# Optimization experiments

Hardware: AMD Instinct MI355X
Metric: run time of the kernel (lower is better)

The kernel has to match this reference:

```python
import jax, jax.numpy as jnp
import numpy as np

N_HIDDEN = 100  # module-level global n_hidden in source
LN_EPS = 1e-5


def _layernorm(x, g, b):
    mu = jnp.mean(x, axis=-1, keepdims=True)
    var = jnp.mean(jnp.square(x - mu), axis=-1, keepdims=True)
    return (x - mu) * jax.lax.rsqrt(var + LN_EPS) * g + b


def setup_inputs() -> dict:
    key = jax.random.key(0)
    B, T, C, H = 8, 1024, 768, 12
    D = C // H  # head_size = 64
    ks = jax.random.split(key, 12)
    s_qkv = 1.0 / np.sqrt(C)
    s_ff1 = 1.0 / np.sqrt(C)
    s_ff2 = 1.0 / np.sqrt(N_HIDDEN)
    return {
        "x": jax.random.normal(ks[0], (B, T, C), dtype=jnp.float32),
        # per-head K/Q/V projections stacked: [H, C, D]
        "Wq": jax.random.uniform(ks[1], (H, C, D), jnp.float32, -s_qkv, s_qkv),
        "Wk": jax.random.uniform(ks[2], (H, C, D), jnp.float32, -s_qkv, s_qkv),
        "Wv": jax.random.uniform(ks[3], (H, C, D), jnp.float32, -s_qkv, s_qkv),
        "Wproj": jax.random.uniform(ks[4], (C, C), jnp.float32, -s_qkv, s_qkv),
        "bproj": jnp.zeros((C,), jnp.float32),
        "ln1_g": jnp.ones((C,), jnp.float32),
        "ln1_b": jnp.zeros((C,), jnp.float32),
        "W1": jax.random.uniform(ks[5], (C, N_HIDDEN), jnp.float32, -s_ff1, s_ff1),
        "b1": jnp.zeros((N_HIDDEN,), jnp.float32),
        "W2": jax.random.uniform(ks[6], (N_HIDDEN, C), jnp.float32, -s_ff2, s_ff2),
        "b2": jnp.zeros((C,), jnp.float32),
        "ln2_g": jnp.ones((C,), jnp.float32),
        "ln2_b": jnp.zeros((C,), jnp.float32),
    }


def reference(x, Wq, Wk, Wv, Wproj, bproj, ln1_g, ln1_b, W1, b1, W2, b2, ln2_g, ln2_b):
    B, T, C = x.shape
    # batched-over-heads QKV (source does a Python loop per head; same math)
    q = jnp.einsum('btc,hcd->bhtd', x, Wq)
    k = jnp.einsum('btc,hcd->bhtd', x, Wk)
    v = jnp.einsum('btc,hcd->bhtd', x, Wv)
    # NOTE: source scales by C**-0.5 where C = n_embd (not head_size)
    wei = jnp.einsum('bhtd,bhsd->bhts', q, k) * (C ** -0.5)
    wei = jax.nn.softmax(wei, axis=-1)  # attn_maps, returned
    out = jnp.einsum('bhts,bhsd->bhtd', wei, v)
    out = out.transpose(0, 2, 1, 3).reshape(B, T, C)  # concat heads
    attn_out = out @ Wproj + bproj
    h = _layernorm(x + attn_out, ln1_g, ln1_b)
    ff = jax.nn.relu(h @ W1 + b1) @ W2 + b2
    y = _layernorm(h + ff, ln2_g, ln2_b)
    return (wei, y)
```

## Files before the change

### kernel.cpp

```cpp
#include <hip/hip_runtime.h>
#include <hip/hip_bf16.h>
#include <cstdint>

typedef __bf16 bf16_t;
typedef __bf16 bf16x8 __attribute__((ext_vector_type(8)));
typedef __bf16 bf16x4 __attribute__((ext_vector_type(4)));
typedef float f32x4 __attribute__((ext_vector_type(4)));

#define B_ 8
#define T_ 1024
#define C_ 768
#define H_ 12
#define D_ 64
#define NTOK 8192
#define NHID_PAD 128
#define SCALE 0.03608439182435161f
#define WEI_ELEMS 100663296ull

__device__ __forceinline__ f32x4 mfma16(bf16x8 a, bf16x8 b, f32x4 c) {
    return __builtin_amdgcn_mfma_f32_16x16x32_bf16(a, b, c, 0, 0, 0);
}

typedef const unsigned int __attribute__((address_space(1)))* gaddr_t;
typedef unsigned int __attribute__((address_space(3)))* laddr_t;
__device__ __forceinline__ void gload16(const bf16_t* g, bf16_t* l) {
    __builtin_amdgcn_global_load_lds((gaddr_t)g, (laddr_t)l, 16, 0, 0);
}

__global__ __launch_bounds__(256) void k_prep(const float* __restrict__ x, bf16_t* __restrict__ xb,
                                              const float* __restrict__ Wq, const float* __restrict__ Wk,
                                              const float* __restrict__ Wv, bf16_t* __restrict__ wqkvt,
                                              const float* __restrict__ Wproj, bf16_t* __restrict__ wprojt,
                                              const float* __restrict__ W1, bf16_t* __restrict__ w1t,
                                              const float* __restrict__ W2, bf16_t* __restrict__ w2t) {
    int blk = blockIdx.x;
    int tid = threadIdx.x;
    if (blk < 6144) {
        int i = blk * 256 + tid;
        const float4 v = reinterpret_cast<const float4*>(x)[i];
        bf16x4 o;
        o.x = (bf16_t)v.x; o.y = (bf16_t)v.y; o.z = (bf16_t)v.z; o.w = (bf16_t)v.w;
        *reinterpret_cast<bf16x4*>(xb + 4 * i) = o;
    } else if (blk < 13056) {
        int idx = (blk - 6144) * 256 + tid;
        int row = idx / C_, c = idx - row * C_;
        int p = row / C_;
        int hd = row - p * C_;
        int h = hd >> 6, d = hd & 63;
        const float* W = (p == 0) ? Wq : (p == 1 ? Wk : Wv);
        wqkvt[idx] = (bf16_t)W[((size_t)h * C_ + c) * D_ + d];
    } else if (blk < 15360) {
        int idx = (blk - 13056) * 256 + tid;
        int n = idx / C_, k = idx - n * C_;
        wprojt[idx] = (bf16_t)Wproj[(size_t)k * C_ + n];
    } else if (blk < 15744) {
        int idx = (blk - 15360) * 256 + tid;
        int n = idx / C_, k = idx - n * C_;
        w1t[idx] = (bf16_t)((n < 100) ? W1[(size_t)k * 100 + n] : 0.0f);
    } else {
        int idx = (blk - 15744) * 256 + tid;
        int n = idx / NHID_PAD, k = idx & (NHID_PAD - 1);
        w2t[idx] = (bf16_t)((k < 100) ? W2[(size_t)k * C_ + n] : 0.0f);
    }
}

__device__ __forceinline__ void gemm_core(bf16_t* As, bf16_t* Bs,
                                          const bf16_t* __restrict__ A, int lda,
                                          const bf16_t* __restrict__ B, int ldb,
                                          int K, int bm, int bn, f32x4 acc[4][4]) {
    const int tid = threadIdx.x;
    const int wave = tid >> 6, lane = tid & 63;
    const int q = lane >> 4, ln = lane & 15;
    const int wm = (wave >> 1) * 64, wn = (wave & 1) * 64;

    const int c0 = wave * 2;
    const int srow = c0 * 16 + (lane >> 2);
    const int kg = (lane & 3) * 8;
    const bf16_t* Ap0 = A + (size_t)(bm + srow) * lda + kg;
    const bf16_t* Ap1 = A + (size_t)(bm + srow + 16) * lda + kg;
    const bf16_t* Bp0 = B + (size_t)(bn + srow) * ldb + kg;
    const bf16_t* Bp1 = B + (size_t)(bn + srow + 16) * ldb + kg;

    const int nt = K >> 5;
    gload16(Ap0, As + c0 * 512);
    gload16(Ap1, As + (c0 + 1) * 512);
    gload16(Bp0, Bs + c0 * 512);
    gload16(Bp1, Bs + (c0 + 1) * 512);
    int cur = 0;
    for (int t = 0; t < nt; ++t) {
        __syncthreads();
        if (t + 1 < nt) {
            int k0 = (t + 1) << 5;
            bf16_t* Ad = As + (cur ^ 1) * 4096;
            bf16_t* Bd = Bs + (cur ^ 1) * 4096;
            gload16(Ap0 + k0, Ad + c0 * 512);
            gload16(Ap1 + k0, Ad + (c0 + 1) * 512);
            gload16(Bp0 + k0, Bd + c0 * 512);
            gload16(Bp1 + k0, Bd + (c0 + 1) * 512);
        }
        const bf16_t* Ab = As + cur * 4096;
        const bf16_t* Bb = Bs + cur * 4096;
        bf16x8 af[4], bfr[4];
#pragma unroll
        for (int i = 0; i < 4; ++i)
            af[i] = *reinterpret_cast<const bf16x8*>(&Ab[(wm + i * 16 + ln) * 32 + q * 8]);
#pragma unroll
        for (int j = 0; j < 4; ++j)
            bfr[j] = *reinterpret_cast<const bf16x8*>(&Bb[(wn + j * 16 + ln) * 32 + q * 8]);
#pragma unroll
        for (int i = 0; i < 4; ++i)
#pragma unroll
            for (int j = 0; j < 4; ++j)
                acc[i][j] = mfma16(af[i], bfr[j], acc[i][j]);
        cur ^= 1;
    }
}

#define EPI_PROLOG(bm, bn)                                      \
    const int lane = threadIdx.x & 63;                          \
    const int wave = threadIdx.x >> 6;                          \
    const int q = lane >> 4, ln = lane & 15;                    \
    const int row0 = (bm) + (wave >> 1) * 64;                   \
    const int col0 = (bn) + (wave & 1) * 64;

__global__ __launch_bounds__(256) void k_gemm_qkv(const bf16_t* __restrict__ xb,
                                                  const bf16_t* __restrict__ wqkvt,
                                                  bf16_t* __restrict__ qb,
                                                  bf16_t* __restrict__ kb,
                                                  bf16_t* __restrict__ vt) {
    __shared__ __align__(16) bf16_t As[2 * 4096];
    __shared__ __align__(16) bf16_t Bs[2 * 4096];
    const int bid = blockIdx.x;
    if (bid < 768) {
        const int bx = bid % 12, by = bid / 12;
        f32x4 acc[4][4] = {};
        gemm_core(As, Bs, xb, C_, wqkvt, C_, C_, by * 128, bx * 128, acc);
        EPI_PROLOG(by * 128, bx * 128)
#pragma unroll
        for (int i = 0; i < 4; ++i)
#pragma unroll
            for (int j = 0; j < 4; ++j)
#pragma unroll
                for (int r = 0; r < 4; ++r) {
                    int grow = row0 + i * 16 + q * 4 + r;
                    int gcol = col0 + j * 16 + ln;
                    int p = (gcol >= C_) ? 1 : 0;
                    int c = gcol - p * C_;
                    int h = c >> 6, d = c & 63;
                    int b = grow >> 10, t = grow & 1023;
                    bf16_t* dst = p ? kb : qb;
                    dst[(((size_t)b * H_ + h) * T_ + t) * D_ + d] = (bf16_t)acc[i][j][r];
                }
    } else {
        const int b2 = bid - 768;
        const int bx = b2 & 63, by = b2 >> 6;
        f32x4 acc[4][4] = {};
        gemm_core(As, Bs, wqkvt + (size_t)1536 * C_, C_, xb, C_, C_, by * 128, bx * 128, acc);
        EPI_PROLOG(by * 128, bx * 128)
#pragma unroll
        for (int i = 0; i < 4; ++i)
#pragma unroll
            for (int j = 0; j < 4; ++j)
#pragma unroll
                for (int r = 0; r < 4; ++r) {
                    int grow = row0 + i * 16 + q * 4 + r;
                    int gcol = col0 + j * 16 + ln;
                    int h = grow >> 6, d = grow & 63;
                    int b = gcol >> 10, t = gcol & 1023;
                    vt[(((size_t)b * H_ + h) * D_ + d) * T_ + t] = (bf16_t)acc[i][j][r];
                }
    }
}

__global__ __launch_bounds__(256) void k_gemm_proj(const bf16_t* __restrict__ A,
                                                   const bf16_t* __restrict__ Bm,
                                                   const float* __restrict__ bias,
                                                   float* __restrict__ out) {
    __shared__ __align__(16) bf16_t As[2 * 4096];
    __shared__ __align__(16) bf16_t Bs[2 * 4096];
    f32x4 acc[4][4] = {};
    gemm_core(As, Bs, A, C_, Bm, C_, C_, blockIdx.y * 128, blockIdx.x * 128, acc);
    EPI_PROLOG(blockIdx.y * 128, blockIdx.x * 128)
#pragma unroll
    for (int i = 0; i < 4; ++i)
#pragma unroll
        for (int j = 0; j < 4; ++j)
#pragma unroll
            for (int r = 0; r < 4; ++r) {
                int grow = row0 + i * 16 + q * 4 + r;
                int gcol = col0 + j * 16 + ln;
                out[(size_t)grow * C_ + gcol] = acc[i][j][r] + bias[gcol];
            }
}

__global__ __launch_bounds__(256) void k_ff(const bf16_t* __restrict__ hbb,
                                            const bf16_t* __restrict__ w1t,
                                            const float* __restrict__ b1,
                                            const bf16_t* __restrict__ w2t,
                                            const float* __restrict__ b2,
                                            float* __restrict__ out) {
    __shared__ __align__(16) bf16_t As[2 * 4096];
    __shared__ __align__(16) bf16_t Bs[2 * 4096];
    __shared__ __align__(16) bf16_t Hs[128 * 128];
    const int bm = blockIdx.y * 128;
    f32x4 acc[4][4] = {};
    gemm_core(As, Bs, hbb, C_, w1t, C_, C_, bm, 0, acc);

    const int tid = threadIdx.x;
    const int wave = tid >> 6, lane = tid & 63;
    const int q = lane >> 4, ln = lane & 15;
    const int wm = (wave >> 1) * 64, wn = (wave & 1) * 64;
#pragma unroll
    for (int i = 0; i < 4; ++i)
#pragma unroll
        for (int j = 0; j < 4; ++j)
#pragma unroll
            for (int r = 0; r < 4; ++r) {
                int row = wm + i * 16 + q * 4 + r;
                int col = wn + j * 16 + ln;
                float v = acc[i][j][r] + ((col < 100) ? b1[col] : 0.0f);
                v = fmaxf(v, 0.0f);
                Hs[(row * 128 + col) ^ ((row & 7) << 3)] = (bf16_t)v;
            }
    __syncthreads();

#pragma unroll
    for (int nt2 = 0; nt2 < 2; ++nt2) {
        const int cb = blockIdx.x * 256 + nt2 * 128;
        f32x4 a2[4][4] = {};
#pragma unroll
        for (int k0 = 0; k0 < 128; k0 += 32) {
            bf16x8 af[4], bfr[4];
#pragma unroll
            for (int i = 0; i < 4; ++i) {
                int row = wm + i * 16 + ln;
                af[i] = *reinterpret_cast<const bf16x8*>(
                    &Hs[(row * 128 + k0 + q * 8) ^ ((row & 7) << 3)]);
            }
#pragma unroll
            for (int j = 0; j < 4; ++j)
                bfr[j] = *reinterpret_cast<const bf16x8*>(
                    &w2t[(size_t)(cb + wn + j * 16 + ln) * NHID_PAD + k0 + q * 8]);
#pragma unroll
            for (int i = 0; i < 4; ++i)
#pragma unroll
                for (int j = 0; j < 4; ++j)
                    a2[i][j] = mfma16(af[i], bfr[j], a2[i][j]);
        }
#pragma unroll
        for (int i = 0; i < 4; ++i)
#pragma unroll
            for (int j = 0; j < 4; ++j)
#pragma unroll
                for (int r = 0; r < 4; ++r) {
                    int grow = bm + wm + i * 16 + q * 4 + r;
                    int gcol = cb + wn + j * 16 + ln;
                    out[(size_t)grow * C_ + gcol] = a2[i][j][r] + b2[gcol];
                }
    }
}

__global__ __launch_bounds__(256, 3) void k_attn(const bf16_t* __restrict__ qb,
                                                 const bf16_t* __restrict__ kb,
                                                 const bf16_t* __restrict__ vt,
                                                 float* __restrict__ wei,
                                                 bf16_t* __restrict__ attn) {
    __shared__ __align__(16) bf16_t Ps[16 * 1032];
    __shared__ float redm[4][16];
    __shared__ float reds[4][16];

    const int tid = threadIdx.x;
    const int w = tid >> 6, lane = tid & 63;
    const int qq = lane >> 4, ln = lane & 15;
    const int bh = blockIdx.y;
    const int b = bh / H_, h = bh - b * H_;
    const int t0 = blockIdx.x * 16;
    const size_t bhbase = (size_t)bh * (T_ * D_);

    const bf16_t* qp = qb + bhbase + (size_t)(t0 + ln) * D_ + qq * 8;
    const bf16x8 aq0 = *reinterpret_cast<const bf16x8*>(qp);
    const bf16x8 aq1 = *reinterpret_cast<const bf16x8*>(qp + 32);

    f32x4 sacc[16] = {};
    const bf16_t* kp = kb + bhbase + (size_t)(w * 256 + ln) * D_ + qq * 8;
#pragma unroll
    for (int j = 0; j < 16; ++j) {
        bf16x8 b0 = *reinterpret_cast<const bf16x8*>(kp + j * 16 * D_);
        bf16x8 b1 = *reinterpret_cast<const bf16x8*>(kp + j * 16 * D_ + 32);
        sacc[j] = mfma16(aq0, b0, sacc[j]);
        sacc[j] = mfma16(aq1, b1, sacc[j]);
    }

    float mx[4];
#pragma unroll
    for (int r = 0; r < 4; ++r) {
        float m = sacc[0][r];
#pragma unroll
        for (int j = 1; j < 16; ++j) m = fmaxf(m, sacc[j][r]);
#pragma unroll
        for (int off = 1; off < 16; off <<= 1) m = fmaxf(m, __shfl_xor(m, off));
        mx[r] = m;
    }
    if (ln == 0) {
#pragma unroll
        for (int r = 0; r < 4; ++r) redm[w][qq * 4 + r] = mx[r];
    }
    __syncthreads();
#pragma unroll
    for (int r = 0; r < 4; ++r) {
        int row = qq * 4 + r;
        mx[r] = fmaxf(fmaxf(redm[0][row], redm[1][row]),
                      fmaxf(redm[2][row], redm[3][row]));
    }

    float rs[4] = {0.0f, 0.0f, 0.0f, 0.0f};
#pragma unroll
    for (int j = 0; j < 16; ++j)
#pragma unroll
        for (int r = 0; r < 4; ++r) {
            float p = __expf((sacc[j][r] - mx[r]) * SCALE);
            sacc[j][r] = p;
            rs[r] += p;
        }
#pragma unroll
    for (int r = 0; r < 4; ++r)
#pragma unroll
        for (int off = 1; off < 16; off <<= 1) rs[r] += __shfl_xor(rs[r], off);
    if (ln == 0) {
#pragma unroll
        for (int r = 0; r < 4; ++r) reds[w][qq * 4 + r] = rs[r];
    }
    __syncthreads();
    float inv[4];
#pragma unroll
    for (int r = 0; r < 4; ++r) {
        int row = qq * 4 + r;
        inv[r] = 1.0f / (reds[0][row] + reds[1][row] + reds[2][row] + reds[3][row]);
    }

    float* wbase = wei + ((size_t)bh << 20) + (size_t)t0 * T_ + w * 256 + ln;
#pragma unroll
    for (int r = 0; r < 4; ++r) {
        int row = qq * 4 + r;
        float* wr = wbase + (size_t)row * T_;
        bf16_t* pr = &Ps[row * 1032 + w * 256 + ln];
#pragma unroll
        for (int j = 0; j < 16; ++j) {
            float p = sacc[j][r] * inv[r];
            __builtin_nontemporal_store(p, wr + j * 16);
            pr[j * 16] = (bf16_t)p;
        }
    }
    __syncthreads();

    f32x4 oacc = {};
    const bf16_t* vp = vt + (size_t)bh * (D_ * T_) + (size_t)(w * 16 + ln) * T_ + qq * 8;
#pragma unroll
    for (int ks = 0; ks < 32; ++ks) {
        bf16x8 a = *reinterpret_cast<const bf16x8*>(&Ps[ln * 1032 + ks * 32 + qq * 8]);
        bf16x8 bv = *reinterpret_cast<const bf16x8*>(vp + ks * 32);
        oacc = mfma16(a, bv, oacc);
    }
#pragma unroll
    for (int r = 0; r < 4; ++r) {
        int trow = t0 + qq * 4 + r;
        attn[((size_t)b * T_ + trow) * C_ + h * D_ + w * 16 + ln] = (bf16_t)oacc[r];
    }
}

__global__ __launch_bounds__(256) void k_ln(const float* __restrict__ a,
                                            const float* __restrict__ bsrc,
                                            const float* __restrict__ g,
                                            const float* __restrict__ beta,
                                            float* __restrict__ of,
                                            bf16_t* __restrict__ ob,
                                            int streaming) {
    int row = blockIdx.x;
    int tid = threadIdx.x;
    const float* pa = a + (size_t)row * C_;
    const float* pb = bsrc + (size_t)row * C_;
    float v[3];
    float s = 0.0f, s2 = 0.0f;
#pragma unroll
    for (int u = 0; u < 3; ++u) {
        int c = tid + u * 256;
        v[u] = pa[c] + pb[c];
        s += v[u];
        s2 += v[u] * v[u];
    }
#pragma unroll
    for (int off = 32; off; off >>= 1) {
        s += __shfl_down(s, off);
        s2 += __shfl_down(s2, off);
    }
    __shared__ float ws[4], ws2[4];
    if ((tid & 63) == 0) { ws[tid >> 6] = s; ws2[tid >> 6] = s2; }
    __syncthreads();
    s = ws[0] + ws[1] + ws[2] + ws[3];
    s2 = ws2[0] + ws2[1] + ws2[2] + ws2[3];
    float mu = s * (1.0f / C_);
    float var = s2 * (1.0f / C_) - mu * mu;
    float ri = rsqrtf(var + 1e-5f);
#pragma unroll
    for (int u = 0; u < 3; ++u) {
        int c = tid + u * 256;
        float y = (v[u] - mu) * ri * g[c] + beta[c];
        if (streaming) __builtin_nontemporal_store(y, &of[(size_t)row * C_ + c]);
        else of[(size_t)row * C_ + c] = y;
        if (ob) ob[(size_t)row * C_ + c] = (bf16_t)y;
    }
}

extern "C" void kernel_launch(void* const* d_in, const int* in_sizes, int n_in,
                              void* d_out, int out_size, void* d_ws, size_t ws_size,
                              hipStream_t stream) {
    const float* x     = (const float*)d_in[0];
    const float* Wq    = (const float*)d_in[1];
    const float* Wk    = (const float*)d_in[2];
    const float* Wv    = (const float*)d_in[3];
    const float* Wproj = (const float*)d_in[4];
    const float* bproj = (const float*)d_in[5];
    const float* ln1g  = (const float*)d_in[6];
    const float* ln1b  = (const float*)d_in[7];
    const float* W1    = (const float*)d_in[8];
    const float* b1    = (const float*)d_in[9];
    const float* W2    = (const float*)d_in[10];
    const float* b2    = (const float*)d_in[11];
    const float* ln2g  = (const float*)d_in[12];
    const float* ln2b  = (const float*)d_in[13];

    char* ws = (char*)d_ws;
    bf16_t* xb     = (bf16_t*)(ws + 0);
    bf16_t* wqkvt  = (bf16_t*)(ws + 12582912);
    bf16_t* qbuf   = (bf16_t*)(ws + 16121856);
    bf16_t* kbuf   = (bf16_t*)(ws + 28704768);
    bf16_t* vtb    = (bf16_t*)(ws + 41287680);
    bf16_t* attnb  = (bf16_t*)(ws + 53870592);
    bf16_t* wprojt = (bf16_t*)(ws + 66453504);
    float*  projb  = (float*)(ws + 67633152);
    float*  hbuf   = (float*)(ws + 92798976);
    bf16_t* w1t    = (bf16_t*)(ws + 120061952);
    bf16_t* w2t    = (bf16_t*)(ws + 120258560);
    bf16_t* hbb    = xb;
    float*  ffb    = projb;

    float* wei = (float*)d_out;
    float* y   = (float*)d_out + WEI_ELEMS;

    k_prep<<<16128, 256, 0, stream>>>(x, xb, Wq, Wk, Wv, wqkvt, Wproj, wprojt,
                                      W1, w1t, W2, w2t);
    k_gemm_qkv<<<1152, 256, 0, stream>>>(xb, wqkvt, qbuf, kbuf, vtb);
    k_attn<<<dim3(64, 96), 256, 0, stream>>>(qbuf, kbuf, vtb, wei, attnb);
    k_gemm_proj<<<dim3(6, 64), 256, 0, stream>>>(attnb, wprojt, bproj, projb);
    k_ln<<<8192, 256, 0, stream>>>(x, projb, ln1g, ln1b, hbuf, hbb, 0);
    k_ff<<<dim3(3, 64), 256, 0, stream>>>(hbb, w1t, b1, w2t, b2, ffb);
    k_ln<<<8192, 256, 0, stream>>>(hbuf, ffb, ln2g, ln2b, y, (bf16_t*)nullptr, 1);

    (void)in_sizes; (void)n_in; (void)out_size; (void)ws_size;
}
```

Baseline: 726.5 us.

## Remap block indices for XCD-local L2 reuse and persist attention blocks over query tiles

Block IDs in the QKV, projection and FF GEMMs are remapped so that consecutive blocks on the same XCD (bid&7) share row panels, aiming to improve per-XCD L2 reuse of A/B tiles. The attention kernel drops from 6144 to 768 blocks, each looping over 8 query tiles of one batch-head, so K/V reuse stays within an XCD's L2. An extra __syncthreads is added in k_ff, presumably to guard LDS reuse. Cost: fewer attention blocks means less parallelism and latency hiding per CU, and loop-carried syncs are added.

```diff
diff --git a/kernel.cpp b/kernel.cpp
--- a/kernel.cpp
+++ b/kernel.cpp
@@ -12,7 +12,6 @@
 #define C_ 768
 #define H_ 12
 #define D_ 64
-#define NTOK 8192
 #define NHID_PAD 128
 #define SCALE 0.03608439182435161f
 #define WEI_ELEMS 100663296ull
@@ -132,7 +131,8 @@
     __shared__ __align__(16) bf16_t Bs[2 * 4096];
     const int bid = blockIdx.x;
     if (bid < 768) {
-        const int bx = bid % 12, by = bid / 12;
+        const int xcd = bid & 7, i2 = bid >> 3;
+        const int by = xcd * 8 + i2 / 12, bx = i2 % 12;
         f32x4 acc[4][4] = {};
         gemm_core(As, Bs, xb, C_, wqkvt, C_, C_, by * 128, bx * 128, acc);
         EPI_PROLOG(by * 128, bx * 128)
@@ -153,7 +153,8 @@
                 }
     } else {
         const int b2 = bid - 768;
-        const int bx = b2 & 63, by = b2 >> 6;
+        const int xcd = b2 & 7, i2 = b2 >> 3;
+        const int bx = xcd * 8 + i2 / 6, by = i2 % 6;
         f32x4 acc[4][4] = {};
         gemm_core(As, Bs, wqkvt + (size_t)1536 * C_, C_, xb, C_, C_, by * 128, bx * 128, acc);
         EPI_PROLOG(by * 128, bx * 128)
@@ -178,9 +179,12 @@
                                                    float* __restrict__ out) {
     __shared__ __align__(16) bf16_t As[2 * 4096];
     __shared__ __align__(16) bf16_t Bs[2 * 4096];
+    const int bid = blockIdx.x;
+    const int xcd = bid & 7, i2 = bid >> 3;
+    const int by = xcd * 8 + i2 / 6, bx = i2 % 6;
     f32x4 acc[4][4] = {};
-    gemm_core(As, Bs, A, C_, Bm, C_, C_, blockIdx.y * 128, blockIdx.x * 128, acc);
-    EPI_PROLOG(blockIdx.y * 128, blockIdx.x * 128)
+    gemm_core(As, Bs, A, C_, Bm, C_, C_, by * 128, bx * 128, acc);
+    EPI_PROLOG(by * 128, bx * 128)
 #pragma unroll
     for (int i = 0; i < 4; ++i)
 #pragma unroll
@@ -202,7 +206,10 @@
     __shared__ __align__(16) bf16_t As[2 * 4096];
     __shared__ __align__(16) bf16_t Bs[2 * 4096];
     __shared__ __align__(16) bf16_t Hs[128 * 128];
-    const int bm = blockIdx.y * 128;
+    const int bid = blockIdx.x;
+    const int xcd = bid & 7, i2 = bid >> 3;
+    const int fy = xcd * 8 + i2 / 3, fx = i2 % 3;
+    const int bm = fy * 128;
     f32x4 acc[4][4] = {};
     gemm_core(As, Bs, hbb, C_, w1t, C_, C_, bm, 0, acc);
 
@@ -210,6 +217,7 @@
     const int wave = tid >> 6, lane = tid & 63;
     const int q = lane >> 4, ln = lane & 15;
     const int wm = (wave >> 1) * 64, wn = (wave & 1) * 64;
+    __syncthreads();
 #pragma unroll
     for (int i = 0; i < 4; ++i)
 #pragma unroll
@@ -226,7 +234,7 @@
 
 #pragma unroll
     for (int nt2 = 0; nt2 < 2; ++nt2) {
-        const int cb = blockIdx.x * 256 + nt2 * 128;
+        const int cb = fx * 256 + nt2 * 128;
         f32x4 a2[4][4] = {};
 #pragma unroll
         for (int k0 = 0; k0 < 128; k0 += 32) {
@@ -272,99 +280,106 @@
     const int tid = threadIdx.x;
     const int w = tid >> 6, lane = tid & 63;
     const int qq = lane >> 4, ln = lane & 15;
-    const int bh = blockIdx.y;
+    const int bid = blockIdx.x;
+    const int tg = bid / 96;
+    const int bh = bid % 96;
     const int b = bh / H_, h = bh - b * H_;
-    const int t0 = blockIdx.x * 16;
     const size_t bhbase = (size_t)bh * (T_ * D_);
 
-    const bf16_t* qp = qb + bhbase + (size_t)(t0 + ln) * D_ + qq * 8;
-    const bf16x8 aq0 = *reinterpret_cast<const bf16x8*>(qp);
-    const bf16x8 aq1 = *reinterpret_cast<const bf16x8*>(qp + 32);
-
-    f32x4 sacc[16] = {};
-    const bf16_t* kp = kb + bhbase + (size_t)(w * 256 + ln) * D_ + qq * 8;
-#pragma unroll
-    for (int j = 0; j < 16; ++j) {
-        bf16x8 b0 = *reinterpret_cast<const bf16x8*>(kp + j * 16 * D_);
-        bf16x8 b1 = *reinterpret_cast<const bf16x8*>(kp + j * 16 * D_ + 32);
-        sacc[j] = mfma16(aq0, b0, sacc[j]);
-        sacc[j] = mfma16(aq1, b1, sacc[j]);
-    }
-
-    float mx[4];
-#pragma unroll
-    for (int r = 0; r < 4; ++r) {
-        float m = sacc[0][r];
-#pragma unroll
-        for (int j = 1; j < 16; ++j) m = fmaxf(m, sacc[j][r]);
-#pragma unroll
-        for (int off = 1; off < 16; off <<= 1) m = fmaxf(m, __shfl_xor(m, off));
-        mx[r] = m;
-    }
-    if (ln == 0) {
-#pragma unroll
-        for (int r = 0; r < 4; ++r) redm[w][qq * 4 + r] = mx[r];
-    }
-    __syncthreads();
-#pragma unroll
-    for (int r = 0; r < 4; ++r) {
-        int row = qq * 4 + r;
-        mx[r] = fmaxf(fmaxf(redm[0][row], redm[1][row]),
-                      fmaxf(redm[2][row], redm[3][row]));
-    }
-
-    float rs[4] = {0.0f, 0.0f, 0.0f, 0.0f};
-#pragma unroll
-    for (int j = 0; j < 16; ++j)
+    for (int u = 0; u < 8; ++u) {
+        const int t0 = (tg * 8 + u) * 16;
+        __syncthreads();
+
+        const bf16_t* qp = qb + bhbase + (size_t)(t0 + ln) * D_ + qq * 8;
+        const bf16x8 aq0 = *reinterpret_cast<const bf16x8*>(qp);
+        const bf16x8 aq1 = *reinterpret_cast<const bf16x8*>(qp + 32);
+
+        f32x4 sacc[16] = {};
+        const bf16_t* kp = kb + bhbase + (size_t)(w * 256 + ln) * D_ + qq * 8;
+#pragma unroll
+        for (int j = 0; j < 16; ++j) {
+            bf16x8 b0 = *reinterpret_cast<const bf16x8*>(kp + j * 16 * D_);
+            bf16x8 b1 = *reinterpret_cast<const bf16x8*>(kp + j * 16 * D_ + 32);
+            sacc[j] = mfma16(aq0, b0, sacc[j]);
+            sacc[j] = mfma16(aq1, b1, sacc[j]);
+        }
+
+        float mx[4];
 #pragma unroll
         for (int r = 0; r < 4; ++r) {
-            float p = __expf((sacc[j][r] - mx[r]) * SCALE);
-            sacc[j][r] = p;
-            rs[r] += p;
-        }
-#pragma unroll
-    for (int r = 0; r < 4; ++r)
-#pragma unroll
-        for (int off = 1; off < 16; off <<= 1) rs[r] += __shfl_xor(rs[r], off);
-    if (ln == 0) {
-#pragma unroll
-        for (int r = 0; r < 4; ++r) reds[w][qq * 4 + r] = rs[r];
-    }
-    __syncthreads();
-    float inv[4];
-#pragma unroll
-    for (int r = 0; r < 4; ++r) {
-        int row = qq * 4 + r;
-        inv[r] = 1.0f / (reds[0][row] + reds[1][row] + reds[2][row] + reds[3][row]);
-    }
-
-    float* wbase = wei + ((size_t)bh << 20) + (size_t)t0 * T_ + w * 256 + ln;
-#pragma unroll
-    for (int r = 0; r < 4; ++r) {
-        int row = qq * 4 + r;
-        float* wr = wbase + (size_t)row * T_;
-        bf16_t* pr = &Ps[row * 1032 + w * 256 + ln];
-#pragma unroll
-        for (int j = 0; j < 16; ++j) {
-            float p = sacc[j][r] * inv[r];
-            __builtin_nontemporal_store(p, wr + j * 16);
-            pr[j * 16] = (bf16_t)p;
-        }
-    }
-    __syncthreads();
-
-    f32x4 oacc = {};
-    const bf16_t* vp = vt + (size_t)bh * (D_ * T_) + (size_t)(w * 16 + ln) * T_ + qq * 8;
-#pragma unroll
-    for (int ks = 0; ks < 32; ++ks) {
-        bf16x8 a = *reinterpret_cast<const bf16x8*>(&Ps[ln * 1032 + ks * 32 + qq * 8]);
-        bf16x8 bv = *reinterpret_cast<const bf16x8*>(vp + ks * 32);
-        oacc = mfma16(a, bv, oacc);
-    }
-#pragma unroll
-    for (int r = 0; r < 4; ++r) {
-        int trow = t0 + qq * 4 + r;
-        attn[((size_t)b * T_ + trow) * C_ + h * D_ + w * 16 + ln] = (bf16_t)oacc[r];
+            float m = sacc[0][r];
+#pragma unroll
+            for (int j = 1; j < 16; ++j) m = fmaxf(m, sacc[j][r]);
+#pragma unroll
+            for (int off = 1; off < 16; off <<= 1) m = fmaxf(m, __shfl_xor(m, off));
+            mx[r] = m;
+        }
+        if (ln == 0) {
+#pragma unroll
+            for (int r = 0; r < 4; ++r) redm[w][qq * 4 + r] = mx[r];
+        }
+        __syncthreads();
+#pragma unroll
+        for (int r = 0; r < 4; ++r) {
+            int row = qq * 4 + r;
+            mx[r] = fmaxf(fmaxf(redm[0][row], redm[1][row]),
+                          fmaxf(redm[2][row], redm[3][row]));
+        }
+
+        float rs[4] = {0.0f, 0.0f, 0.0f, 0.0f};
+#pragma unroll
+        for (int j = 0; j < 16; ++j)
+#pragma unroll
+            for (int r = 0; r < 4; ++r) {
+                float p = __expf((sacc[j][r] - mx[r]) * SCALE);
+                sacc[j][r] = p;
+                rs[r] += p;
+            }
+#pragma unroll
+        for (int r = 0; r < 4; ++r)
+#pragma unroll
+            for (int off = 1; off < 16; off <<= 1) rs[r] += __shfl_xor(rs[r], off);
+        if (ln == 0) {
+#pragma unroll
+            for (int r = 0; r < 4; ++r) reds[w][qq * 4 + r] = rs[r];
+        }
+        __syncthreads();
+        float inv[4];
+#pragma unroll
+        for (int r = 0; r < 4; ++r) {
+            int row = qq * 4 + r;
+            inv[r] = 1.0f / (reds[0][row] + reds[1][row] +
+                             reds[2][row] + reds[3][row]);
+        }
+
+        float* wbase = wei + ((size_t)bh << 20) + (size_t)t0 * T_ + w * 256 + ln;
+#pragma unroll
+        for (int r = 0; r < 4; ++r) {
+            int row = qq * 4 + r;
+            float* wr = wbase + (size_t)row * T_;
+            bf16_t* pr = &Ps[row * 1032 + w * 256 + ln];
+#pragma unroll
+            for (int j = 0; j < 16; ++j) {
+                float p = sacc[j][r] * inv[r];
+                __builtin_nontemporal_store(p, wr + j * 16);
+                pr[j * 16] = (bf16_t)p;
+            }
+        }
+        __syncthreads();
+
+        f32x4 oacc = {};
+        const bf16_t* vp = vt + (size_t)bh * (D_ * T_) + (size_t)(w * 16 + ln) * T_ + qq * 8;
+#pragma unroll
+        for (int ks = 0; ks < 32; ++ks) {
+            bf16x8 a = *reinterpret_cast<const bf16x8*>(&Ps[ln * 1032 + ks * 32 + qq * 8]);
+            bf16x8 bv = *reinterpret_cast<const bf16x8*>(vp + ks * 32);
+            oacc = mfma16(a, bv, oacc);
+        }
+#pragma unroll
+        for (int r = 0; r < 4; ++r) {
+            int trow = t0 + qq * 4 + r;
+            attn[((size_t)b * T_ + trow) * C_ + h * D_ + w * 16 + ln] = (bf16_t)oacc[r];
+        }
     }
 }
 
@@ -450,10 +465,10 @@
     k_prep<<<16128, 256, 0, stream>>>(x, xb, Wq, Wk, Wv, wqkvt, Wproj, wprojt,
                                       W1, w1t, W2, w2t);
     k_gemm_qkv<<<1152, 256, 0, stream>>>(xb, wqkvt, qbuf, kbuf, vtb);
-    k_attn<<<dim3(64, 96), 256, 0, stream>>>(qbuf, kbuf, vtb, wei, attnb);
-    k_gemm_proj<<<dim3(6, 64), 256, 0, stream>>>(attnb, wprojt, bproj, projb);
+    k_attn<<<768, 256, 0, stream>>>(qbuf, kbuf, vtb, wei, attnb);
+    k_gemm_proj<<<384, 256, 0, stream>>>(attnb, wprojt, bproj, projb);
     k_ln<<<8192, 256, 0, stream>>>(x, projb, ln1g, ln1b, hbuf, hbb, 0);
-    k_ff<<<dim3(3, 64), 256, 0, stream>>>(hbb, w1t, b1, w2t, b2, ffb);
+    k_ff<<<192, 256, 0, stream>>>(hbb, w1t, b1, w2t, b2, ffb);
     k_ln<<<8192, 256, 0, stream>>>(hbuf, ffb, ln2g, ln2b, y, (bf16_t*)nullptr, 1);
 
     (void)in_sizes; (void)n_in; (void)out_size; (void)ws_size;
```

After: 865.2 us. 19.1% more time.
